# Performance work log

Measured on AMD Instinct MI355X. Metric: run time of the kernel, lower is better.

Reference implementation:

```python
import jax, jax.numpy as jnp
import numpy as np

NX, DX, H, DO = 8192, 8, 1024, 1


def setup_inputs() -> dict:
    key = jax.random.key(0)
    ks = jax.random.split(key, 7)
    s1 = 1.0 / np.sqrt(DX)  # torch Linear default init bound
    s2 = 1.0 / np.sqrt(H)
    x = jax.random.normal(ks[0], (NX, DX), jnp.float32)
    W1 = jax.random.uniform(ks[1], (H, DX), jnp.float32, -s1, s1)
    b1 = jax.random.uniform(ks[2], (H,), jnp.float32, -s1, s1)
    W2 = jax.random.uniform(ks[3], (H, H), jnp.float32, -s2, s2)
    b2 = jax.random.uniform(ks[4], (H,), jnp.float32, -s2, s2)
    W3 = jax.random.uniform(ks[5], (DO, H), jnp.float32, -s2, s2)
    b3 = jax.random.uniform(ks[6], (DO,), jnp.float32, -s2, s2)
    return {"x": x, "W1": W1, "b1": b1, "W2": W2, "b2": b2, "W3": W3, "b3": b3}


def reference(x, W1, b1, W2, b2, W3, b3):
    # Forward: Linear -> Tanh -> Linear -> Tanh -> Linear
    z1 = jnp.tanh(x @ W1.T + b1)          # [nx, h]
    z2 = jnp.tanh(z1 @ W2.T + b2)         # [nx, h]
    y = z2 @ W3.T + b3                    # [nx, out]

    # DerivTanh(h) = 4/(e^-h + e^h)^2 = sech^2(h) = 1 - tanh(h)^2
    d1 = 1.0 - z1 * z1                    # [nx, h]
    d2 = 1.0 - z2 * z2                    # [nx, h]

    # Vectorized analytic Jacobian (original loops over each input dim k):
    # tmp_k = d2 * (W2 @ (d1 * W1[:, k]))  then  dydx_k = W3 @ tmp_k
    J = d1[:, :, None] * W1[None, :, :]                    # [nx, h, dx]
    J = d2[:, :, None] * jnp.einsum('ij,njk->nik', W2, J)  # [nx, h, dx]
    dydx = jnp.einsum('oj,njk->nok', W3, J)                # [nx, out, dx]
    # Match original list-of-dx ordering: dydx[k] has shape [nx, out]
    dydx = jnp.transpose(dydx, (2, 0, 1))                  # [dx, nx, out]
    return y, dydx
```

## Files before the change

kernel.cpp:

```cpp
#include <hip/hip_runtime.h>
#include <stdint.h>

#define NXS 8192
#define HS  1024

typedef __attribute__((ext_vector_type(8))) short short8;
typedef __attribute__((ext_vector_type(4))) float f32x4;

__device__ __forceinline__ float bf2f(uint32_t b) {
    union { uint32_t u; float f; } c; c.u = b << 16; return c.f;
}
__device__ __forceinline__ uint16_t f2bf(float f) {
    union { float f; uint32_t u; } c; c.f = f;
    return (uint16_t)((c.u + 0x7fffu + ((c.u >> 16) & 1u)) >> 16);
}
__device__ __forceinline__ void async_cp16(const void* g, void* l) {
    __builtin_amdgcn_global_load_lds(
        (const __attribute__((address_space(1))) void*)g,
        (__attribute__((address_space(3))) void*)l,
        16, 0, 0);
}

__global__ __launch_bounds__(256) void k01(
    const float* __restrict__ x, const float* __restrict__ W1,
    const float* __restrict__ b1, const float* __restrict__ W2,
    const float* __restrict__ b3, uint16_t* __restrict__ Z1,
    uint16_t* __restrict__ Bp1, uint16_t* __restrict__ Bp2,
    uint16_t* __restrict__ W1T, float* __restrict__ out)
{
    __shared__ float xs[8][8];
    const int b = blockIdx.x, t = threadIdx.x;
    if (b < 1024) {
        const int n0 = b * 8;
        if (t < 64) xs[t >> 3][t & 7] = x[n0 * 8 + t];
        const int j = t * 4;
        float w[4][8];
#pragma unroll
        for (int c = 0; c < 4; ++c) {
            float4 w0 = *(const float4*)(W1 + (j + c) * 8);
            float4 w1 = *(const float4*)(W1 + (j + c) * 8 + 4);
            w[c][0] = w0.x; w[c][1] = w0.y; w[c][2] = w0.z; w[c][3] = w0.w;
            w[c][4] = w1.x; w[c][5] = w1.y; w[c][6] = w1.z; w[c][7] = w1.w;
        }
        float4 bb = *(const float4*)(b1 + j);
        const float bv[4] = {bb.x, bb.y, bb.z, bb.w};
        __syncthreads();
#pragma unroll
        for (int s = 0; s < 8; ++s) {
            ushort4 o;
            uint16_t* op = (uint16_t*)&o;
#pragma unroll
            for (int c = 0; c < 4; ++c) {
                float sum = bv[c];
#pragma unroll
                for (int k = 0; k < 8; ++k) sum += xs[s][k] * w[c][k];
                op[c] = f2bf(tanhf(sum));
            }
            *(ushort4*)(Z1 + (size_t)(n0 + s) * HS + j) = o;
        }
    } else if (b < 1536) {
        const int tid = (b - 1024) * 256 + t;
        const int l = tid & 63, c = (tid >> 6) & 31, g = tid >> 11;
        const int lr = l & 15, lq = l >> 4;
        const float* src = W2 + (size_t)(g * 16 + lr) * HS + c * 32 + lq * 8;
        float4 a0 = *(const float4*)src;
        float4 a1 = *(const float4*)(src + 4);
        uint16_t o[8];
        o[0] = f2bf(a0.x); o[1] = f2bf(a0.y); o[2] = f2bf(a0.z); o[3] = f2bf(a0.w);
        o[4] = f2bf(a1.x); o[5] = f2bf(a1.y); o[6] = f2bf(a1.z); o[7] = f2bf(a1.w);
        *(ushort4*)(Bp1 + (size_t)tid * 8)     = *(ushort4*)&o[0];
        *(ushort4*)(Bp1 + (size_t)tid * 8 + 4) = *(ushort4*)&o[4];
    } else if (b < 2048) {
        const int tid = (b - 1536) * 256 + t;
        const int l = tid & 63, c = (tid >> 6) & 31, g = tid >> 11;
        const int lr = l & 15, lq = l >> 4;
        uint16_t o[8];
#pragma unroll
        for (int j2 = 0; j2 < 8; ++j2)
            o[j2] = f2bf(W2[(size_t)(c * 32 + lq * 8 + j2) * HS + g * 16 + lr]);
        *(ushort4*)(Bp2 + (size_t)tid * 8)     = *(ushort4*)&o[0];
        *(ushort4*)(Bp2 + (size_t)tid * 8 + 4) = *(ushort4*)&o[4];
    } else if (b < 2336) {
        const int idx = (b - 2048) * 256 + t;
        out[idx] = (idx < NXS) ? b3[0] : 0.f;
    } else {
        const int idx = (b - 2336) * 256 + t;
        const int r = idx >> 10, cc = idx & 1023;
        W1T[idx] = (r < 8) ? f2bf(W1[cc * 8 + r]) : (uint16_t)0;
    }
}

template <int MODE>
__global__ __launch_bounds__(256, 2) void gemm_k(
    const uint16_t* __restrict__ A, const uint16_t* __restrict__ Bp,
    const float* __restrict__ bias, const float* __restrict__ W3,
    uint16_t* __restrict__ Out, float* __restrict__ yOut,
    const uint16_t* __restrict__ Z1, const uint16_t* __restrict__ W1T,
    float* __restrict__ dOut)
{
    __shared__ __attribute__((aligned(16))) uint16_t smem[32768];
    const int t = threadIdx.x;
    const int wave = t >> 6, lane = t & 63;
    const int lq = lane >> 4, lr = lane & 15;
    const int wr = wave >> 1, wc = wave & 1;
    const int rowBase = blockIdx.x * 128;
    const int colBase = blockIdx.y * 128;

    const uint16_t* gA[4];
#pragma unroll
    for (int i = 0; i < 4; ++i) {
        int s = t + i * 256;
        int rA = s >> 3, qA = (s & 7) ^ (rA & 7);
        gA[i] = A + (size_t)(rowBase + rA) * HS + qA * 8;
    }
    const uint16_t* gB[4];
#pragma unroll
    for (int i = 0; i < 4; ++i) {
        int s = t + i * 256;
        gB[i] = Bp + ((size_t)(colBase >> 4) + (s >> 7)) * 16384
                   + (size_t)((s >> 6) & 1) * 512 + (size_t)(s & 63) * 8;
    }

    f32x4 acc[4][4] = {};

#pragma unroll
    for (int i = 0; i < 4; ++i)
        async_cp16(gA[i], (char*)smem + t * 16 + i * 4096);
#pragma unroll
    for (int i = 0; i < 4; ++i)
        async_cp16(gB[i], (char*)smem + 32768 + t * 16 + i * 4096);
    __syncthreads();

    int buf = 0;
    for (int c = 0; c < 16; ++c) {
        if (c < 15) {
#pragma unroll
            for (int i = 0; i < 4; ++i)
                async_cp16(gA[i] + (c + 1) * 64,
                           (char*)smem + (buf ^ 1) * 16384 + t * 16 + i * 4096);
#pragma unroll
            for (int i = 0; i < 4; ++i)
                async_cp16(gB[i] + (c + 1) * 1024,
                           (char*)smem + 32768 + (buf ^ 1) * 16384 + t * 16 + i * 4096);
        }
        const uint16_t* pA  = smem + buf * 8192;
        const uint16_t* pBl = smem + 16384 + buf * 8192;
#pragma unroll
        for (int kk = 0; kk < 2; ++kk) {
            short8 bfrag[4];
#pragma unroll
            for (int tj = 0; tj < 4; ++tj)
                bfrag[tj] = *(const short8*)(pBl
                    + (((wc * 4 + tj) * 2 + kk) * 64 + lane) * 8);
            short8 af[4];
#pragma unroll
            for (int ti = 0; ti < 4; ++ti) {
                int ar = wr * 64 + ti * 16 + lr;
                af[ti] = *(const short8*)(pA + ar * 64
                          + ((((kk << 2) + lq) ^ (ar & 7)) << 3));
            }
#pragma unroll
            for (int ti = 0; ti < 4; ++ti)
#pragma unroll
                for (int tj = 0; tj < 4; ++tj)
                    acc[ti][tj] = __builtin_amdgcn_mfma_f32_16x16x32_bf16(
                        af[ti], bfrag[tj], acc[ti][tj], 0, 0, 0);
        }
        __syncthreads();
        buf ^= 1;
    }

    if (MODE == 0) {
        float cB[4], cW[4]; int cCol[4];
#pragma unroll
        for (int tj = 0; tj < 4; ++tj) {
            cCol[tj] = colBase + wc * 64 + tj * 16 + lr;
            cB[tj] = bias[cCol[tj]];
            cW[tj] = W3[cCol[tj]];
        }
#pragma unroll
        for (int ti = 0; ti < 4; ++ti) {
#pragma unroll
            for (int r = 0; r < 4; ++r) {
                int row = rowBase + wr * 64 + ti * 16 + lq * 4 + r;
                float ys = 0.f;
#pragma unroll
                for (int tj = 0; tj < 4; ++tj) {
                    float z2 = tanhf(acc[ti][tj][r] + cB[tj]);
                    ys += z2 * cW[tj];
                    Out[(size_t)row * HS + cCol[tj]] = f2bf((1.f - z2 * z2) * cW[tj]);
                }
                ys += __shfl_xor(ys, 1); ys += __shfl_xor(ys, 2);
                ys += __shfl_xor(ys, 4); ys += __shfl_xor(ys, 8);
                if (lr == 0) atomicAdd(&yOut[row], ys);
            }
        }
    } else {
#pragma unroll
        for (int ti = 0; ti < 4; ++ti)
#pragma unroll
            for (int r = 0; r < 4; ++r) {
                int rowl = wr * 64 + ti * 16 + lq * 4 + r;
                const size_t zrow = (size_t)(rowBase + rowl) * HS + colBase;
#pragma unroll
                for (int tj = 0; tj < 4; ++tj) {
                    int coll = wc * 64 + tj * 16 + lr;
                    float z1 = bf2f(Z1[zrow + coll]);
                    smem[rowl * 136 + coll] =
                        f2bf(acc[ti][tj][r] * (1.f - z1 * z1));
                }
            }
        __syncthreads();
        f32x4 dd[2] = {};
#pragma unroll
        for (int h = 0; h < 2; ++h)
#pragma unroll
            for (int kb = 0; kb < 4; ++kb) {
                short8 aF = *(const short8*)(smem + (wave * 32 + h * 16 + lr) * 136
                                             + kb * 32 + lq * 8);
                short8 bF = *(const short8*)(W1T + (size_t)lr * HS + colBase
                                             + kb * 32 + lq * 8);
                dd[h] = __builtin_amdgcn_mfma_f32_16x16x32_bf16(aF, bF, dd[h], 0, 0, 0);
            }
        if (lr < 8) {
#pragma unroll
            for (int h = 0; h < 2; ++h) {
                int row = rowBase + wave * 32 + h * 16 + lq * 4;
#pragma unroll
                for (int rg = 0; rg < 4; ++rg)
                    atomicAdd(&dOut[(size_t)lr * NXS + row + rg], dd[h][rg]);
            }
        }
    }
}

extern "C" void kernel_launch(void* const* d_in, const int* in_sizes, int n_in,
                              void* d_out, int out_size, void* d_ws, size_t ws_size,
                              hipStream_t stream) {
    (void)in_sizes; (void)n_in; (void)out_size; (void)ws_size;
    const float* x  = (const float*)d_in[0];
    const float* W1 = (const float*)d_in[1];
    const float* b1 = (const float*)d_in[2];
    const float* W2 = (const float*)d_in[3];
    const float* b2 = (const float*)d_in[4];
    const float* W3 = (const float*)d_in[5];
    const float* b3 = (const float*)d_in[6];
    float* out = (float*)d_out;

    char* ws = (char*)d_ws;
    uint16_t* Z1  = (uint16_t*)(ws);
    uint16_t* V   = (uint16_t*)(ws + (size_t)16 * 1024 * 1024);
    uint16_t* Bp1 = (uint16_t*)(ws + (size_t)32 * 1024 * 1024);
    uint16_t* Bp2 = (uint16_t*)(ws + (size_t)34 * 1024 * 1024);
    uint16_t* W1T = (uint16_t*)(ws + (size_t)36 * 1024 * 1024);

    k01<<<2400, 256, 0, stream>>>(x, W1, b1, W2, b3, Z1, Bp1, Bp2, W1T, out);
    gemm_k<0><<<dim3(NXS / 128, HS / 128), 256, 0, stream>>>(
        Z1, Bp1, b2, W3, V, out, nullptr, nullptr, nullptr);
    gemm_k<1><<<dim3(NXS / 128, HS / 128), 256, 0, stream>>>(
        V, Bp2, nullptr, nullptr, nullptr, nullptr, Z1, W1T, out + NXS);
}
```

Before: 134.6 us.

## Use 3-stage K=32 LDS pipeline with vmcnt waits and fast tanh

Replaces the double-buffered K=64 GEMM main loop with a triple-buffered K=32 pipeline. It uses explicit s_waitcnt vmcnt and raw s_barrier so that two tiles stay in flight while one is consumed, and the A-tile swizzle is adjusted to the narrower rows. LDS use drops from 64KB to 48KB per block. Separately, tanhf is replaced with an exp-based fast_tanh in the Z1 and Z2 epilogues, which trades some accuracy for fewer instructions. The finer K step doubles the number of barriers and halves the MFMA work done between them.

Result: no change. 132.2 us (-1.8%).

```diff
diff --git a/kernel.cpp b/kernel.cpp
--- a/kernel.cpp
+++ b/kernel.cpp
@@ -13,6 +13,10 @@
 __device__ __forceinline__ uint16_t f2bf(float f) {
     union { float f; uint32_t u; } c; c.f = f;
     return (uint16_t)((c.u + 0x7fffu + ((c.u >> 16) & 1u)) >> 16);
+}
+__device__ __forceinline__ float fast_tanh(float x) {
+    float xc = fminf(fmaxf(x, -15.f), 15.f);
+    return 1.f - __fdividef(2.f, __expf(2.f * xc) + 1.f);
 }
 __device__ __forceinline__ void async_cp16(const void* g, void* l) {
     __builtin_amdgcn_global_load_lds(
@@ -54,7 +58,7 @@
                 float sum = bv[c];
 #pragma unroll
                 for (int k = 0; k < 8; ++k) sum += xs[s][k] * w[c][k];
-                op[c] = f2bf(tanhf(sum));
+                op[c] = f2bf(fast_tanh(sum));
             }
             *(ushort4*)(Z1 + (size_t)(n0 + s) * HS + j) = o;
         }
@@ -98,7 +102,7 @@
     const uint16_t* __restrict__ Z1, const uint16_t* __restrict__ W1T,
     float* __restrict__ dOut)
 {
-    __shared__ __attribute__((aligned(16))) uint16_t smem[32768];
+    __shared__ __attribute__((aligned(16))) uint16_t smem[24576];
     const int t = threadIdx.x;
     const int wave = t >> 6, lane = t & 63;
     const int lq = lane >> 4, lr = lane & 15;
@@ -106,68 +110,80 @@
     const int rowBase = blockIdx.x * 128;
     const int colBase = blockIdx.y * 128;
 
-    const uint16_t* gA[4];
-#pragma unroll
-    for (int i = 0; i < 4; ++i) {
-        int s = t + i * 256;
-        int rA = s >> 3, qA = (s & 7) ^ (rA & 7);
-        gA[i] = A + (size_t)(rowBase + rA) * HS + qA * 8;
-    }
-    const uint16_t* gB[4];
-#pragma unroll
-    for (int i = 0; i < 4; ++i) {
-        int s = t + i * 256;
-        gB[i] = Bp + ((size_t)(colBase >> 4) + (s >> 7)) * 16384
-                   + (size_t)((s >> 6) & 1) * 512 + (size_t)(s & 63) * 8;
-    }
+    const uint16_t* gA0;
+    const uint16_t* gA1;
+    {
+        int s0 = t,       r0 = s0 >> 2, q0 = (s0 & 3) ^ ((r0 >> 1) & 3);
+        int s1 = t + 256, r1 = s1 >> 2, q1 = (s1 & 3) ^ ((r1 >> 1) & 3);
+        gA0 = A + (size_t)(rowBase + r0) * HS + q0 * 8;
+        gA1 = A + (size_t)(rowBase + r1) * HS + q1 * 8;
+    }
+    const uint16_t* gB0;
+    const uint16_t* gB1;
+    {
+        int s0 = t,       s1 = t + 256;
+        gB0 = Bp + ((size_t)(colBase >> 4) + (s0 >> 6)) * 16384 + (size_t)(s0 & 63) * 8;
+        gB1 = Bp + ((size_t)(colBase >> 4) + (s1 >> 6)) * 16384 + (size_t)(s1 & 63) * 8;
+    }
+    const int ldsA0 = t * 16;
+    const int ldsA1 = t * 16 + 4096;
+    const int ldsB0 = t * 16 + 8192;
+    const int ldsB1 = t * 16 + 12288;
 
     f32x4 acc[4][4] = {};
 
-#pragma unroll
-    for (int i = 0; i < 4; ++i)
-        async_cp16(gA[i], (char*)smem + t * 16 + i * 4096);
-#pragma unroll
-    for (int i = 0; i < 4; ++i)
-        async_cp16(gB[i], (char*)smem + 32768 + t * 16 + i * 4096);
-    __syncthreads();
-
-    int buf = 0;
-    for (int c = 0; c < 16; ++c) {
-        if (c < 15) {
-#pragma unroll
-            for (int i = 0; i < 4; ++i)
-                async_cp16(gA[i] + (c + 1) * 64,
-                           (char*)smem + (buf ^ 1) * 16384 + t * 16 + i * 4096);
-#pragma unroll
-            for (int i = 0; i < 4; ++i)
-                async_cp16(gB[i] + (c + 1) * 1024,
-                           (char*)smem + 32768 + (buf ^ 1) * 16384 + t * 16 + i * 4096);
-        }
-        const uint16_t* pA  = smem + buf * 8192;
-        const uint16_t* pBl = smem + 16384 + buf * 8192;
-#pragma unroll
-        for (int kk = 0; kk < 2; ++kk) {
-            short8 bfrag[4];
+    async_cp16(gA0,       (char*)smem + ldsA0);
+    async_cp16(gA1,       (char*)smem + ldsA1);
+    async_cp16(gB0,       (char*)smem + ldsB0);
+    async_cp16(gB1,       (char*)smem + ldsB1);
+    async_cp16(gA0 + 32,  (char*)smem + 16384 + ldsA0);
+    async_cp16(gA1 + 32,  (char*)smem + 16384 + ldsA1);
+    async_cp16(gB0 + 512, (char*)smem + 16384 + ldsB0);
+    async_cp16(gB1 + 512, (char*)smem + 16384 + ldsB1);
+    gA0 += 64; gA1 += 64; gB0 += 1024; gB1 += 1024;
+    asm volatile("s_waitcnt vmcnt(4)" ::: "memory");
+    __builtin_amdgcn_s_barrier();
+
+    int rb = 0;
+    int wb = 2;
+#pragma unroll 1
+    for (int c = 0; c < 32; ++c) {
+        if (c < 30) {
+            char* d = (char*)smem + wb * 16384;
+            async_cp16(gA0, d + ldsA0);
+            async_cp16(gA1, d + ldsA1);
+            async_cp16(gB0, d + ldsB0);
+            async_cp16(gB1, d + ldsB1);
+            gA0 += 32; gA1 += 32; gB0 += 512; gB1 += 512;
+            asm volatile("" ::: "memory");
+        }
+        const uint16_t* pA  = smem + rb * 8192;
+        const uint16_t* pBl = pA + 4096;
+        short8 bfrag[4];
+#pragma unroll
+        for (int tj = 0; tj < 4; ++tj)
+            bfrag[tj] = *(const short8*)(pBl + (((wc << 2) + tj) * 64 + lane) * 8);
+        short8 af[4];
+#pragma unroll
+        for (int ti = 0; ti < 4; ++ti) {
+            int ar = wr * 64 + ti * 16 + lr;
+            af[ti] = *(const short8*)(pA + ar * 32
+                      + ((lq ^ ((ar >> 1) & 3)) << 3));
+        }
+#pragma unroll
+        for (int ti = 0; ti < 4; ++ti)
 #pragma unroll
             for (int tj = 0; tj < 4; ++tj)
-                bfrag[tj] = *(const short8*)(pBl
-                    + (((wc * 4 + tj) * 2 + kk) * 64 + lane) * 8);
-            short8 af[4];
-#pragma unroll
-            for (int ti = 0; ti < 4; ++ti) {
-                int ar = wr * 64 + ti * 16 + lr;
-                af[ti] = *(const short8*)(pA + ar * 64
-                          + ((((kk << 2) + lq) ^ (ar & 7)) << 3));
-            }
-#pragma unroll
-            for (int ti = 0; ti < 4; ++ti)
-#pragma unroll
-                for (int tj = 0; tj < 4; ++tj)
-                    acc[ti][tj] = __builtin_amdgcn_mfma_f32_16x16x32_bf16(
-                        af[ti], bfrag[tj], acc[ti][tj], 0, 0, 0);
-        }
-        __syncthreads();
-        buf ^= 1;
+                acc[ti][tj] = __builtin_amdgcn_mfma_f32_16x16x32_bf16(
+                    af[ti], bfrag[tj], acc[ti][tj], 0, 0, 0);
+        if (c < 30) {
+            asm volatile("s_waitcnt vmcnt(4)" ::: "memory");
+        } else {
+            asm volatile("s_waitcnt vmcnt(0)" ::: "memory");
+        }
+        __builtin_amdgcn_s_barrier();
+        rb = (rb == 2) ? 0 : rb + 1;
+        wb = (wb == 2) ? 0 : wb + 1;
     }
 
     if (MODE == 0) {
@@ -186,7 +202,7 @@
                 float ys = 0.f;
 #pragma unroll
                 for (int tj = 0; tj < 4; ++tj) {
-                    float z2 = tanhf(acc[ti][tj][r] + cB[tj]);
+                    float z2 = fast_tanh(acc[ti][tj][r] + cB[tj]);
                     ys += z2 * cW[tj];
                     Out[(size_t)row * HS + cCol[tj]] = f2bf((1.f - z2 * z2) * cW[tj]);
                 }
```
